# Kernel optimization log

Measured on AMD Instinct MI355X. Metric: run time of the kernel, lower is better.

The kernel has to match this reference:

```python
import jax, jax.numpy as jnp
import numpy as np

B, L, D, H = 4, 2048, 1024, 64  # batch, seq, d_model, head_size

def setup_inputs() -> dict:
    key = jax.random.key(0)
    k1, k2 = jax.random.split(key)
    x = jax.random.normal(k1, (B, L, D), dtype=jnp.float32)
    # nn.Linear(d_model, head_size, bias=False) weight: [head_size, d_model]
    Wq = jax.random.normal(k2, (H, D), dtype=jnp.float32) * (1.0 / np.sqrt(D))
    return {"x": x, "Wq": Wq}

def reference(x, Wq):
    # Faithful to source bug: q, k, v ALL use the query projection.
    q = jnp.einsum('bld,hd->blh', x, Wq)
    k = q
    v = q
    d_k = x.shape[-1]  # source uses d_model, not head_size
    scores = jnp.einsum('blh,bmh->blm', q, k) / jnp.sqrt(jnp.float32(d_k))
    Lq = x.shape[1]
    causal = jnp.tril(jnp.ones((Lq, Lq), dtype=bool))
    scores = jnp.where(causal, scores, -jnp.inf)
    attn = jax.nn.softmax(scores, axis=-1)
    # dropout in eval mode -> identity
    return jnp.einsum('blm,bmh->blh', attn, v)
```

## Files before the change

kernel.cpp:

```cpp
#include <hip/hip_runtime.h>
#include <cmath>

#define Bb 4
#define Ll 2048
#define Dd 1024
#define Hh 64

typedef float f32x4 __attribute__((ext_vector_type(4)));
typedef short s16x8 __attribute__((ext_vector_type(8)));

__device__ __forceinline__ unsigned short f2bf(float f) {
    union { float f; unsigned int u; } v; v.f = f;
    unsigned int u = v.u;
    return (unsigned short)((u + 0x7FFFu + ((u >> 16) & 1u)) >> 16);
}
__device__ __forceinline__ unsigned int pack2(float a, float b) {
    return (unsigned int)f2bf(a) | ((unsigned int)f2bf(b) << 16);
}

__global__ __launch_bounds__(256) void proj_mfma(const float* __restrict__ x,
                                                 const float* __restrict__ Wq,
                                                 unsigned short* __restrict__ q,
                                                 unsigned short* __restrict__ qT) {
    __shared__ uint4 xs4[16 * 16];
    __shared__ uint4 ws4[16 * 64];
    const int t = threadIdx.x;
    const int lane = t & 63;
    const int w = t >> 6;
    const int m15 = lane & 15;
    const int q_ = lane >> 4;
    const int row0 = blockIdx.x * 16;

    f32x4 acc = {0.f, 0.f, 0.f, 0.f};
    const int rx = t >> 4, kcx = t & 15;

    for (int k0 = 0; k0 < Dd; k0 += 128) {
        __syncthreads();
        {
            const float* src = x + (size_t)(row0 + rx) * Dd + k0 + kcx * 8;
            float4 a = *(const float4*)src;
            float4 b = *(const float4*)(src + 4);
            uint4 p; p.x = pack2(a.x, a.y); p.y = pack2(a.z, a.w);
            p.z = pack2(b.x, b.y); p.w = pack2(b.z, b.w);
            xs4[kcx * 16 + (rx ^ kcx)] = p;
        }
#pragma unroll
        for (int j = 0; j < 4; ++j) {
            int idx = t + j * 256;
            int h = idx >> 4, kc = idx & 15;
            const float* src = Wq + (size_t)h * Dd + k0 + kc * 8;
            float4 a = *(const float4*)src;
            float4 b = *(const float4*)(src + 4);
            uint4 p; p.x = pack2(a.x, a.y); p.y = pack2(a.z, a.w);
            p.z = pack2(b.x, b.y); p.w = pack2(b.z, b.w);
            ws4[kc * 64 + (h ^ kc)] = p;
        }
        __syncthreads();
        const int hB = w * 16 + m15;
#pragma unroll
        for (int ks = 0; ks < 4; ++ks) {
            int kc = ks * 4 + q_;
            s16x8 A = *(const s16x8*)&xs4[kc * 16 + (m15 ^ kc)];
            s16x8 B = *(const s16x8*)&ws4[kc * 64 + (hB ^ kc)];
            acc = __builtin_amdgcn_mfma_f32_16x16x32_bf16(A, B, acc, 0, 0, 0);
        }
    }
    const int h = w * 16 + m15;
    const int b = row0 >> 11;
    const int mloc = (row0 & 2047) + q_ * 4;
    unsigned short u0 = f2bf(acc[0]), u1 = f2bf(acc[1]), u2 = f2bf(acc[2]), u3 = f2bf(acc[3]);
    q[(size_t)(row0 + q_ * 4 + 0) * Hh + h] = u0;
    q[(size_t)(row0 + q_ * 4 + 1) * Hh + h] = u1;
    q[(size_t)(row0 + q_ * 4 + 2) * Hh + h] = u2;
    q[(size_t)(row0 + q_ * 4 + 3) * Hh + h] = u3;
    ushort4 pk; pk.x = u0; pk.y = u1; pk.z = u2; pk.w = u3;
    *(ushort4*)&qT[((size_t)(b * Hh + h)) * Ll + mloc] = pk;
}

__global__ __launch_bounds__(256) void flash_mfma(const unsigned short* __restrict__ qg,
                                                  const unsigned short* __restrict__ qTg,
                                                  float* __restrict__ PO,
                                                  float* __restrict__ ML) {
    const int qt = blockIdx.x;
    const int s  = blockIdx.y;
    const int b  = blockIdx.z;
    if (s > (qt >> 2)) return;
    __shared__ uint4 Qs4[512], Ks4[512], Vt4[512];
    __shared__ __align__(16) unsigned short Pb[4 * 128 * 8];
    const int t = threadIdx.x, lane = t & 63, w = t >> 6;
    const int m15 = lane & 15, q_ = lane >> 4;
    const unsigned short* qb  = qg  + (size_t)b * Ll * Hh;
    const unsigned short* qTb = qTg + (size_t)b * Hh * Ll;

#pragma unroll
    for (int j = 0; j < 2; ++j) {
        int idx = t + j * 256;
        int r = idx >> 3, hc = idx & 7;
        Qs4[hc * 64 + (r ^ hc)] = *(const uint4*)(qb + (size_t)(qt * 64 + r) * Hh + hc * 8);
    }
    f32x4 Oacc[4];
    float mr[4], lr[4];
#pragma unroll
    for (int i = 0; i < 4; ++i) {
        Oacc[i] = (f32x4){0.f, 0.f, 0.f, 0.f};
        mr[i] = -INFINITY; lr[i] = 0.f;
    }
    const int n_it = min(4, qt - 4 * s + 1);
    const int c_base = s * 256;

    for (int it = 0; it < n_it; ++it) {
        const int c0 = c_base + it * 64;
        __syncthreads();
#pragma unroll
        for (int j = 0; j < 2; ++j) {
            int idx = t + j * 256;
            int c = idx >> 3, hc = idx & 7;
            Ks4[hc * 64 + (c ^ hc)] = *(const uint4*)(qb + (size_t)(c0 + c) * Hh + hc * 8);
        }
#pragma unroll
        for (int j = 0; j < 2; ++j) {
            int idx = t + j * 256;
            int h = idx >> 3, cc = idx & 7;
            Vt4[cc * 64 + (h ^ cc)] = *(const uint4*)(qTb + (size_t)h * Ll + c0 + cc * 8);
        }
        __syncthreads();
        f32x4 sc[4];
#pragma unroll
        for (int ct = 0; ct < 4; ++ct) sc[ct] = (f32x4){0.f, 0.f, 0.f, 0.f};
#pragma unroll
        for (int ks = 0; ks < 2; ++ks) {
            int hc = ks * 4 + q_;
            s16x8 A = *(const s16x8*)&Qs4[hc * 64 + ((w * 16 + m15) ^ hc)];
#pragma unroll
            for (int ct = 0; ct < 4; ++ct) {
                s16x8 Bk = *(const s16x8*)&Ks4[hc * 64 + ((ct * 16 + m15) ^ hc)];
                sc[ct] = __builtin_amdgcn_mfma_f32_16x16x32_bf16(A, Bk, sc[ct], 0, 0, 0);
            }
        }
        const bool diag = (4 * s + it) == qt;
#pragma unroll
        for (int r = 0; r < 4; ++r) {
            const int row = qt * 64 + w * 16 + q_ * 4 + r;
            float v[4];
#pragma unroll
            for (int ct = 0; ct < 4; ++ct) {
                float sv = sc[ct][r] * 0.03125f;
                if (diag && (c0 + ct * 16 + m15 > row)) sv = -INFINITY;
                v[ct] = sv;
            }
            float vmax = fmaxf(fmaxf(v[0], v[1]), fmaxf(v[2], v[3]));
            vmax = fmaxf(vmax, __shfl_xor(vmax, 1, 64));
            vmax = fmaxf(vmax, __shfl_xor(vmax, 2, 64));
            vmax = fmaxf(vmax, __shfl_xor(vmax, 4, 64));
            vmax = fmaxf(vmax, __shfl_xor(vmax, 8, 64));
            float mnew = fmaxf(mr[r], vmax);
            float alpha = __expf(mr[r] - mnew);
            float psum = 0.f;
#pragma unroll
            for (int ct = 0; ct < 4; ++ct) {
                float p = __expf(v[ct] - mnew);
                psum += p;
                int c = ct * 16 + m15, cc = c >> 3;
                Pb[(w * 128 + cc * 16 + ((q_ * 4 + r) ^ cc)) * 8 + (c & 7)] = f2bf(p);
            }
            psum += __shfl_xor(psum, 1, 64);
            psum += __shfl_xor(psum, 2, 64);
            psum += __shfl_xor(psum, 4, 64);
            psum += __shfl_xor(psum, 8, 64);
            lr[r] = lr[r] * alpha + psum;
            mr[r] = mnew;
#pragma unroll
            for (int ht = 0; ht < 4; ++ht) Oacc[ht][r] *= alpha;
        }
#pragma unroll
        for (int ks = 0; ks < 2; ++ks) {
            int cc = ks * 4 + q_;
            s16x8 Ap = *(const s16x8*)&Pb[(w * 128 + cc * 16 + (m15 ^ cc)) * 8];
#pragma unroll
            for (int ht = 0; ht < 4; ++ht) {
                s16x8 Bv = *(const s16x8*)&Vt4[cc * 64 + ((ht * 16 + m15) ^ cc)];
                Oacc[ht] = __builtin_amdgcn_mfma_f32_16x16x32_bf16(Ap, Bv, Oacc[ht], 0, 0, 0);
            }
        }
    }
    const size_t base = ((size_t)((b * 32 + qt) * 8 + s)) * 4096;
#pragma unroll
    for (int ht = 0; ht < 4; ++ht)
#pragma unroll
        for (int r = 0; r < 4; ++r)
            PO[base + (size_t)(w * 16 + q_ * 4 + r) * 64 + ht * 16 + m15] = Oacc[ht][r];
    if (m15 == 0) {
        float* mlp = ML + ((size_t)((b * 32 + qt) * 8 + s)) * 128;
#pragma unroll
        for (int r = 0; r < 4; ++r) {
            mlp[(w * 16 + q_ * 4 + r) * 2 + 0] = mr[r];
            mlp[(w * 16 + q_ * 4 + r) * 2 + 1] = lr[r];
        }
    }
}

__global__ __launch_bounds__(256) void combine_k(const float* __restrict__ PO,
                                                 const float* __restrict__ ML,
                                                 float* __restrict__ out) {
    const int bq = blockIdx.x;
    const int b = bq >> 5, qt = bq & 31;
    const int ns = (qt >> 2) + 1;
    const int t = threadIdx.x;
    const int r = blockIdx.y * 32 + (t >> 3);
    const int c8 = (t & 7) * 8;
    const float* mlp = ML + (size_t)bq * 8 * 128;
    const float* pob = PO + (size_t)bq * 8 * 4096;
    float M = -INFINITY;
    for (int si = 0; si < ns; ++si) M = fmaxf(M, mlp[si * 128 + r * 2]);
    float L = 0.f;
    f32x4 a0 = {0.f, 0.f, 0.f, 0.f}, a1 = a0;
    for (int si = 0; si < ns; ++si) {
        float ms = mlp[si * 128 + r * 2], ls = mlp[si * 128 + r * 2 + 1];
        float wgt = __expf(ms - M);
        L += ls * wgt;
        const f32x4* sp = (const f32x4*)(pob + (size_t)si * 4096 + r * 64 + c8);
        a0 += wgt * sp[0];
        a1 += wgt * sp[1];
    }
    float inv = 1.0f / L;
    f32x4* op = (f32x4*)(out + (size_t)(b * Ll + qt * 64 + r) * 64 + c8);
    op[0] = a0 * inv;
    op[1] = a1 * inv;
}

extern "C" void kernel_launch(void* const* d_in, const int* in_sizes, int n_in,
                              void* d_out, int out_size, void* d_ws, size_t ws_size,
                              hipStream_t stream) {
    const float* x  = (const float*)d_in[0];
    const float* Wq = (const float*)d_in[1];
    float* out = (float*)d_out;
    char* ws = (char*)d_ws;
    unsigned short* q  = (unsigned short*)ws;
    unsigned short* qT = (unsigned short*)(ws + (1 << 20));
    float* PO = (float*)(ws + (2 << 20));
    float* ML = (float*)(ws + (18 << 20));

    proj_mfma<<<512, 256, 0, stream>>>(x, Wq, q, qT);
    flash_mfma<<<dim3(32, 8, Bb), 256, 0, stream>>>(q, qT, PO, ML);
    combine_k<<<dim3(128, 2), 256, 0, stream>>>(PO, ML, out);
}
```

Measured before the change: 118.7 us.

## Pre-convert Wq to bf16, widen proj K-step, transpose flash MFMA operand roles

A new small kernel converts Wq to bf16 once per call, so the projection kernel loads bf16 weights directly instead of converting them in every block. The projection also uses a 256-wide K chunk with larger shared tiles and a launch-bounds occupancy hint. In the flash kernel, the MFMA operands are swapped so each lane owns one query row, which turns the softmax row reductions into mostly in-register work with only two shuffles and lets P be written with packed stores and O stored as vectors. This adds an extra launch and workspace buffer and changes register pressure under the new occupancy hints.

```diff
diff --git a/kernel.cpp b/kernel.cpp
--- a/kernel.cpp
+++ b/kernel.cpp
@@ -18,12 +18,22 @@
     return (unsigned int)f2bf(a) | ((unsigned int)f2bf(b) << 16);
 }
 
-__global__ __launch_bounds__(256) void proj_mfma(const float* __restrict__ x,
-                                                 const float* __restrict__ Wq,
-                                                 unsigned short* __restrict__ q,
-                                                 unsigned short* __restrict__ qT) {
-    __shared__ uint4 xs4[16 * 16];
-    __shared__ uint4 ws4[16 * 64];
+__global__ __launch_bounds__(256) void wq_cvt(const float* __restrict__ Wq,
+                                              unsigned short* __restrict__ wqb) {
+    const int i = (blockIdx.x * 256 + threadIdx.x) * 8;
+    float4 a = *(const float4*)(Wq + i);
+    float4 b = *(const float4*)(Wq + i + 4);
+    uint4 p; p.x = pack2(a.x, a.y); p.y = pack2(a.z, a.w);
+    p.z = pack2(b.x, b.y); p.w = pack2(b.z, b.w);
+    *(uint4*)(wqb + i) = p;
+}
+
+__global__ __launch_bounds__(256, 2) void proj_mfma(const float* __restrict__ x,
+                                                    const unsigned short* __restrict__ wqb,
+                                                    unsigned short* __restrict__ q,
+                                                    unsigned short* __restrict__ qT) {
+    __shared__ uint4 xs4[32 * 16];
+    __shared__ uint4 ws4[32 * 64];
     const int t = threadIdx.x;
     const int lane = t & 63;
     const int w = t >> 6;
@@ -32,36 +42,32 @@
     const int row0 = blockIdx.x * 16;
 
     f32x4 acc = {0.f, 0.f, 0.f, 0.f};
-    const int rx = t >> 4, kcx = t & 15;
-
-    for (int k0 = 0; k0 < Dd; k0 += 128) {
-        __syncthreads();
-        {
-            const float* src = x + (size_t)(row0 + rx) * Dd + k0 + kcx * 8;
+
+    for (int k0 = 0; k0 < Dd; k0 += 256) {
+        __syncthreads();
+#pragma unroll
+        for (int j = 0; j < 2; ++j) {
+            int idx = t + j * 256;
+            int r = idx >> 5, kc = idx & 31;
+            const float* src = x + (size_t)(row0 + r) * Dd + k0 + kc * 8;
             float4 a = *(const float4*)src;
             float4 b = *(const float4*)(src + 4);
             uint4 p; p.x = pack2(a.x, a.y); p.y = pack2(a.z, a.w);
             p.z = pack2(b.x, b.y); p.w = pack2(b.z, b.w);
-            xs4[kcx * 16 + (rx ^ kcx)] = p;
-        }
-#pragma unroll
-        for (int j = 0; j < 4; ++j) {
-            int idx = t + j * 256;
-            int h = idx >> 4, kc = idx & 15;
-            const float* src = Wq + (size_t)h * Dd + k0 + kc * 8;
-            float4 a = *(const float4*)src;
-            float4 b = *(const float4*)(src + 4);
-            uint4 p; p.x = pack2(a.x, a.y); p.y = pack2(a.z, a.w);
-            p.z = pack2(b.x, b.y); p.w = pack2(b.z, b.w);
-            ws4[kc * 64 + (h ^ kc)] = p;
-        }
-        __syncthreads();
-        const int hB = w * 16 + m15;
-#pragma unroll
-        for (int ks = 0; ks < 4; ++ks) {
+            xs4[kc * 16 + (r ^ (kc & 15))] = p;
+        }
+#pragma unroll
+        for (int j = 0; j < 8; ++j) {
+            int idx = t + j * 256;
+            int h = idx >> 5, kc = idx & 31;
+            ws4[kc * 64 + (h ^ kc)] = *(const uint4*)(wqb + (size_t)h * Dd + k0 + kc * 8);
+        }
+        __syncthreads();
+#pragma unroll
+        for (int ks = 0; ks < 8; ++ks) {
             int kc = ks * 4 + q_;
-            s16x8 A = *(const s16x8*)&xs4[kc * 16 + (m15 ^ kc)];
-            s16x8 B = *(const s16x8*)&ws4[kc * 64 + (hB ^ kc)];
+            s16x8 A = *(const s16x8*)&xs4[kc * 16 + (m15 ^ (kc & 15))];
+            s16x8 B = *(const s16x8*)&ws4[kc * 64 + ((w * 16 + m15) ^ kc)];
             acc = __builtin_amdgcn_mfma_f32_16x16x32_bf16(A, B, acc, 0, 0, 0);
         }
     }
@@ -77,16 +83,16 @@
     *(ushort4*)&qT[((size_t)(b * Hh + h)) * Ll + mloc] = pk;
 }
 
-__global__ __launch_bounds__(256) void flash_mfma(const unsigned short* __restrict__ qg,
-                                                  const unsigned short* __restrict__ qTg,
-                                                  float* __restrict__ PO,
-                                                  float* __restrict__ ML) {
+__global__ __launch_bounds__(256, 3) void flash_mfma(const unsigned short* __restrict__ qg,
+                                                     const unsigned short* __restrict__ qTg,
+                                                     float* __restrict__ PO,
+                                                     float* __restrict__ ML) {
     const int qt = blockIdx.x;
     const int s  = blockIdx.y;
     const int b  = blockIdx.z;
     if (s > (qt >> 2)) return;
     __shared__ uint4 Qs4[512], Ks4[512], Vt4[512];
-    __shared__ __align__(16) unsigned short Pb[4 * 128 * 8];
+    __shared__ __align__(16) unsigned short Pb[4 * 16 * 72];
     const int t = threadIdx.x, lane = t & 63, w = t >> 6;
     const int m15 = lane & 15, q_ = lane >> 4;
     const unsigned short* qb  = qg  + (size_t)b * Ll * Hh;
@@ -99,14 +105,13 @@
         Qs4[hc * 64 + (r ^ hc)] = *(const uint4*)(qb + (size_t)(qt * 64 + r) * Hh + hc * 8);
     }
     f32x4 Oacc[4];
-    float mr[4], lr[4];
-#pragma unroll
-    for (int i = 0; i < 4; ++i) {
-        Oacc[i] = (f32x4){0.f, 0.f, 0.f, 0.f};
-        mr[i] = -INFINITY; lr[i] = 0.f;
-    }
+#pragma unroll
+    for (int i = 0; i < 4; ++i) Oacc[i] = (f32x4){0.f, 0.f, 0.f, 0.f};
+    float mr = -INFINITY, lr = 0.f;
     const int n_it = min(4, qt - 4 * s + 1);
     const int c_base = s * 256;
+    const int row = qt * 64 + w * 16 + m15;
+    unsigned short* Pr = Pb + (w * 16 + m15) * 72;
 
     for (int it = 0; it < n_it; ++it) {
         const int c0 = c_base + it * 64;
@@ -130,72 +135,65 @@
 #pragma unroll
         for (int ks = 0; ks < 2; ++ks) {
             int hc = ks * 4 + q_;
-            s16x8 A = *(const s16x8*)&Qs4[hc * 64 + ((w * 16 + m15) ^ hc)];
+            s16x8 Bq = *(const s16x8*)&Qs4[hc * 64 + ((w * 16 + m15) ^ hc)];
 #pragma unroll
             for (int ct = 0; ct < 4; ++ct) {
-                s16x8 Bk = *(const s16x8*)&Ks4[hc * 64 + ((ct * 16 + m15) ^ hc)];
-                sc[ct] = __builtin_amdgcn_mfma_f32_16x16x32_bf16(A, Bk, sc[ct], 0, 0, 0);
+                s16x8 Ak = *(const s16x8*)&Ks4[hc * 64 + ((ct * 16 + m15) ^ hc)];
+                sc[ct] = __builtin_amdgcn_mfma_f32_16x16x32_bf16(Ak, Bq, sc[ct], 0, 0, 0);
             }
         }
         const bool diag = (4 * s + it) == qt;
-#pragma unroll
-        for (int r = 0; r < 4; ++r) {
-            const int row = qt * 64 + w * 16 + q_ * 4 + r;
-            float v[4];
-#pragma unroll
-            for (int ct = 0; ct < 4; ++ct) {
+        float v[16];
+#pragma unroll
+        for (int ct = 0; ct < 4; ++ct)
+#pragma unroll
+            for (int r = 0; r < 4; ++r) {
                 float sv = sc[ct][r] * 0.03125f;
-                if (diag && (c0 + ct * 16 + m15 > row)) sv = -INFINITY;
-                v[ct] = sv;
+                if (diag && (c0 + ct * 16 + q_ * 4 + r > row)) sv = -INFINITY;
+                v[ct * 4 + r] = sv;
             }
-            float vmax = fmaxf(fmaxf(v[0], v[1]), fmaxf(v[2], v[3]));
-            vmax = fmaxf(vmax, __shfl_xor(vmax, 1, 64));
-            vmax = fmaxf(vmax, __shfl_xor(vmax, 2, 64));
-            vmax = fmaxf(vmax, __shfl_xor(vmax, 4, 64));
-            vmax = fmaxf(vmax, __shfl_xor(vmax, 8, 64));
-            float mnew = fmaxf(mr[r], vmax);
-            float alpha = __expf(mr[r] - mnew);
-            float psum = 0.f;
-#pragma unroll
-            for (int ct = 0; ct < 4; ++ct) {
-                float p = __expf(v[ct] - mnew);
-                psum += p;
-                int c = ct * 16 + m15, cc = c >> 3;
-                Pb[(w * 128 + cc * 16 + ((q_ * 4 + r) ^ cc)) * 8 + (c & 7)] = f2bf(p);
+        float vmax = v[0];
+#pragma unroll
+        for (int i = 1; i < 16; ++i) vmax = fmaxf(vmax, v[i]);
+        vmax = fmaxf(vmax, __shfl_xor(vmax, 16, 64));
+        vmax = fmaxf(vmax, __shfl_xor(vmax, 32, 64));
+        float mnew = fmaxf(mr, vmax);
+        float alpha = __expf(mr - mnew);
+        float p[16];
+        float psum = 0.f;
+#pragma unroll
+        for (int i = 0; i < 16; ++i) { p[i] = __expf(v[i] - mnew); psum += p[i]; }
+        psum += __shfl_xor(psum, 16, 64);
+        psum += __shfl_xor(psum, 32, 64);
+        lr = lr * alpha + psum;
+        mr = mnew;
+#pragma unroll
+        for (int ht = 0; ht < 4; ++ht) Oacc[ht] *= alpha;
+#pragma unroll
+        for (int ct = 0; ct < 4; ++ct) {
+            uint2 pr; pr.x = pack2(p[ct * 4 + 0], p[ct * 4 + 1]);
+            pr.y = pack2(p[ct * 4 + 2], p[ct * 4 + 3]);
+            *(uint2*)(Pr + ct * 16 + q_ * 4) = pr;
+        }
+#pragma unroll
+        for (int kc = 0; kc < 2; ++kc) {
+            int cc = kc * 4 + q_;
+            s16x8 Bp = *(const s16x8*)(Pr + kc * 32 + q_ * 8);
+#pragma unroll
+            for (int ht = 0; ht < 4; ++ht) {
+                s16x8 Av = *(const s16x8*)&Vt4[cc * 64 + ((ht * 16 + m15) ^ cc)];
+                Oacc[ht] = __builtin_amdgcn_mfma_f32_16x16x32_bf16(Av, Bp, Oacc[ht], 0, 0, 0);
             }
-            psum += __shfl_xor(psum, 1, 64);
-            psum += __shfl_xor(psum, 2, 64);
-            psum += __shfl_xor(psum, 4, 64);
-            psum += __shfl_xor(psum, 8, 64);
-            lr[r] = lr[r] * alpha + psum;
-            mr[r] = mnew;
-#pragma unroll
-            for (int ht = 0; ht < 4; ++ht) Oacc[ht][r] *= alpha;
-        }
-#pragma unroll
-        for (int ks = 0; ks < 2; ++ks) {
-            int cc = ks * 4 + q_;
-            s16x8 Ap = *(const s16x8*)&Pb[(w * 128 + cc * 16 + (m15 ^ cc)) * 8];
-#pragma unroll
-            for (int ht = 0; ht < 4; ++ht) {
-                s16x8 Bv = *(const s16x8*)&Vt4[cc * 64 + ((ht * 16 + m15) ^ cc)];
-                Oacc[ht] = __builtin_amdgcn_mfma_f32_16x16x32_bf16(Ap, Bv, Oacc[ht], 0, 0, 0);
-            }
         }
     }
     const size_t base = ((size_t)((b * 32 + qt) * 8 + s)) * 4096;
 #pragma unroll
     for (int ht = 0; ht < 4; ++ht)
-#pragma unroll
-        for (int r = 0; r < 4; ++r)
-            PO[base + (size_t)(w * 16 + q_ * 4 + r) * 64 + ht * 16 + m15] = Oacc[ht][r];
-    if (m15 == 0) {
+        *(f32x4*)&PO[base + (size_t)(w * 16 + m15) * 64 + ht * 16 + q_ * 4] = Oacc[ht];
+    if (q_ == 0) {
         float* mlp = ML + ((size_t)((b * 32 + qt) * 8 + s)) * 128;
-#pragma unroll
-        for (int r = 0; r < 4; ++r) {
-            mlp[(w * 16 + q_ * 4 + r) * 2 + 0] = mr[r];
-            mlp[(w * 16 + q_ * 4 + r) * 2 + 1] = lr[r];
-        }
+        mlp[(w * 16 + m15) * 2 + 0] = mr;
+        mlp[(w * 16 + m15) * 2 + 1] = lr;
     }
 }
 
@@ -235,12 +233,14 @@
     const float* Wq = (const float*)d_in[1];
     float* out = (float*)d_out;
     char* ws = (char*)d_ws;
-    unsigned short* q  = (unsigned short*)ws;
-    unsigned short* qT = (unsigned short*)(ws + (1 << 20));
+    unsigned short* q   = (unsigned short*)ws;
+    unsigned short* qT  = (unsigned short*)(ws + (1 << 20));
     float* PO = (float*)(ws + (2 << 20));
     float* ML = (float*)(ws + (18 << 20));
-
-    proj_mfma<<<512, 256, 0, stream>>>(x, Wq, q, qT);
+    unsigned short* wqb = (unsigned short*)(ws + (19 << 20));
+
+    wq_cvt<<<32, 256, 0, stream>>>(Wq, wqb);
+    proj_mfma<<<512, 256, 0, stream>>>(x, wqb, q, qT);
     flash_mfma<<<dim3(32, 8, Bb), 256, 0, stream>>>(q, qT, PO, ML);
     combine_k<<<dim3(128, 2), 256, 0, stream>>>(PO, ML, out);
 }
```

Result: faster. 101.6 us (-14.4%).
